# Performance work log

Hardware: AMD Instinct MI355X
Metric: run time of the kernel (lower is better)

The kernel has to match this reference:

```python
import jax, jax.numpy as jnp
import numpy as np

A = 16          # n_agents
H = 128         # rnn_hidden_dim
IN = 128        # input_shape
NA = 32         # n_attention
NACT = 14       # n_actions
TAU = 0.5       # gumbel_softmax_tau
B_ENV = 1024    # parallel envs
BZ = B_ENV * A

# neighbor index: for agent i, all j != i (matches select_ind in torch code)
IDX = np.array([[j for j in range(A) if j != i] for i in range(A)])  # [A, A-1]


def gru_cell(x, h, Wih, Whh, bih, bhh):
    # torch GRUCell gate order: r, z, n
    gi = x @ Wih.T + bih
    gh = h @ Whh.T + bhh
    ir, iz, inn = jnp.split(gi, 3, axis=-1)
    hr, hz, hn = jnp.split(gh, 3, axis=-1)
    r = jax.nn.sigmoid(ir + hr)
    z = jax.nn.sigmoid(iz + hz)
    n = jnp.tanh(inn + r * hn)
    return (1.0 - z) * n + z * h


def run_gru(seq, Wih, Whh, bih, bhh):
    # seq: [T, N, D]; returns all hidden states [T, N, H]
    h0 = jnp.zeros((seq.shape[1], Whh.shape[1]), seq.dtype)
    def step(h, x):
        h2 = gru_cell(x, h, Wih, Whh, bih, bhh)
        return h2, h2
    _, ys = jax.lax.scan(step, h0, seq)
    return ys


def setup_inputs() -> dict:
    key = jax.random.key(0)
    ks = jax.random.split(key, 24)
    def u(k, shape, fan):
        s = 1.0 / np.sqrt(fan)
        return jax.random.uniform(k, shape, jnp.float32, -s, s)
    inp = {
        "inputs": jax.random.normal(ks[0], (BZ, IN), jnp.float32),
        "hidden_state": jax.random.normal(ks[1], (BZ, H), jnp.float32),
        "gumbel_u": jax.random.uniform(ks[2], (BZ * (A - 1), 2), jnp.float32),
        # fc1
        "W1": u(ks[3], (H, IN), IN), "b1": u(ks[4], (H,), IN),
        # GRUCell
        "Wih_c": u(ks[5], (3 * H, H), H), "Whh_c": u(ks[6], (3 * H, H), H),
        "bih_c": u(ks[7], (3 * H,), H), "bhh_c": u(ks[8], (3 * H,), H),
        # bi-GRU forward dir (input 2H)
        "Wih_f": u(ks[9], (3 * H, 2 * H), H), "Whh_f": u(ks[10], (3 * H, H), H),
        "bih_f": u(ks[11], (3 * H,), H), "bhh_f": u(ks[12], (3 * H,), H),
        # bi-GRU backward dir
        "Wih_b": u(ks[13], (3 * H, 2 * H), H), "Whh_b": u(ks[14], (3 * H, H), H),
        "bih_b": u(ks[15], (3 * H,), H), "bhh_b": u(ks[16], (3 * H,), H),
        # hard classifier
        "Wc": u(ks[17], (2, 2 * H), 2 * H), "bc": u(ks[18], (2,), 2 * H),
        # attention projections (no bias)
        "Wq": u(ks[19], (NA, H), H), "Wk": u(ks[20], (NA, H), H),
        # fc2
        "W2": u(ks[21], (NACT, 2 * H), 2 * H), "b2": u(ks[22], (NACT,), 2 * H),
    }
    return inp


def reference(inputs, hidden_state, gumbel_u, W1, b1, Wih_c, Whh_c, bih_c, bhh_c,
              Wih_f, Whh_f, bih_f, bhh_f, Wih_b, Whh_b, bih_b, bhh_b,
              Wc, bc, Wq, Wk, W2, b2):
    bz = inputs.shape[0]
    B = bz // A
    x1 = jax.nn.relu(inputs @ W1.T + b1)
    h_rnn = gru_cell(x1, hidden_state.reshape(-1, H), Wih_c, Whh_c, bih_c, bhh_c)  # [bz, H]

    h3 = h_rnn.reshape(B, A, H)
    nbr = h3[:, IDX, :]                                           # [B, A, A-1, H]
    self_rep = jnp.broadcast_to(h3[:, :, None, :], (B, A, A - 1, H))
    pairs = jnp.concatenate([self_rep, nbr], axis=-1)             # [B, A, A-1, 2H]
    seq = pairs.transpose(2, 0, 1, 3).reshape(A - 1, bz, 2 * H)   # [T, bz, 2H]

    yf = run_gru(seq, Wih_f, Whh_f, bih_f, bhh_f)
    yb = jnp.flip(run_gru(jnp.flip(seq, 0), Wih_b, Whh_b, bih_b, bhh_b), 0)
    h_hard = jnp.concatenate([yf, yb], axis=-1)                   # [T, bz, 2H]
    h_hard = h_hard.transpose(1, 0, 2).reshape(-1, 2 * H)         # [bz*T, 2H]

    logits = h_hard @ Wc.T + bc                                   # [bz*T, 2]
    g = -jnp.log(-jnp.log(gumbel_u + 1e-10) + 1e-10)
    gs = jax.nn.softmax((logits + g) / TAU, axis=-1)
    hard_w = gs[:, 1].reshape(B, A, A - 1)                        # hard gate

    q = (h_rnn @ Wq.T).reshape(B, A, NA)
    k = (h_rnn @ Wk.T).reshape(B, A, NA)
    kn = k[:, IDX, :] * hard_w[..., None]                         # [B, A, A-1, NA]
    scores = jnp.einsum('bad,bamd->bam', q, kn) / np.sqrt(NA)
    soft_w = jax.nn.softmax(scores, axis=-1)                      # [B, A, A-1]

    w = hard_w * soft_w
    agg = jnp.einsum('bam,bamh->bah', w, nbr).reshape(bz, H)
    out = jnp.concatenate([h_rnn, agg], axis=-1) @ W2.T + b2      # [bz, n_actions]
    return out, h_rnn
```

## Files before the change

kernel.cpp:

```cpp
#include <hip/hip_runtime.h>
#include <hip/hip_bf16.h>


typedef __attribute__((ext_vector_type(8))) short short8;
typedef __attribute__((ext_vector_type(4))) float float4v;

#define BF2F(x) __bfloat162float(x)
typedef __hip_bfloat16 bf;

__device__ __forceinline__ float frcp(float x) {
  return __builtin_amdgcn_rcpf(x);
}
__device__ __forceinline__ float fsigmoid(float x) {
  return frcp(1.f + __expf(-x));
}
__device__ __forceinline__ float ftanh(float x) {
  float e = __expf(2.f * x);
  return 1.f - 2.f * frcp(1.f + e);
}
__device__ __forceinline__ float rdv(const void* p, int i, int f) {
  return f ? ((const float*)p)[i] : BF2F(((const bf*)p)[i]);
}
__device__ __forceinline__ float upk(unsigned long long v, int s) {
  union { unsigned int i; float f; } x;
  x.i = ((unsigned int)((v >> s) & 0xffffULL)) << 16;
  return x.f;
}

static const int AO[23] = {
  0, 2097152, 4194304, 4685824, 4702208, 4702336, 4751488, 4800640, 4801024,
  4801408, 4899712, 4948864, 4949248, 4949632, 5047936, 5097088, 5097472,
  5097856, 5098368, 5098384, 5102480, 5106576, 5110160};
static const int AN[23] = {
  2097152, 2097152, 491520, 16384, 128, 49152, 49152, 384, 384, 98304, 49152,
  384, 384, 98304, 49152, 384, 384, 512, 2, 4096, 4096, 3584, 14};

struct CArgs {
  const void* src[23];
  int n[23];
  int off[23];
};

__global__ void kDetect(const unsigned short* __restrict__ p, int* flag) {
  __shared__ int s;
  if (threadIdx.x == 0) s = 0;
  __syncthreads();
  int hit = 0;
  for (int i = threadIdx.x; i < 4096; i += 1024) {
    int e = (p[i] >> 7) & 0xFF;
    if (e >= 0xC0) hit = 1;
  }
  if (hit) atomicOr(&s, 1);
  __syncthreads();
  if (threadIdx.x == 0) *flag = s;
}

__global__ void kConvert(CArgs a, const int* __restrict__ flag,
                         bf* __restrict__ arena) {
  const int b = blockIdx.y;
  const int n = a.n[b];
  const int f = *flag;
  bf* dst = arena + a.off[b];
  if (f) {
    const float* s = (const float*)a.src[b];
    for (int i = blockIdx.x * 256 + threadIdx.x; i < n; i += gridDim.x * 256)
      dst[i] = __float2bfloat16(s[i]);
  } else {
    const unsigned short* s = (const unsigned short*)a.src[b];
    unsigned short* d = (unsigned short*)dst;
    for (int i = blockIdx.x * 256 + threadIdx.x; i < n; i += gridDim.x * 256)
      d[i] = s[i];
  }
}

__global__ void kPrep(const bf* __restrict__ Wq, const bf* __restrict__ Wk,
                      const bf* __restrict__ W2a, const bf* __restrict__ WcA,
                      bf* __restrict__ Wqk, bf* __restrict__ W2p,
                      bf* __restrict__ Wcb) {
  int idx = blockIdx.x * 256 + threadIdx.x;
  if (idx < 8192) {
    int r = idx >> 7, c = idx & 127;
    Wqk[idx] = (r < 32) ? Wq[r * 128 + c] : Wk[(r - 32) * 128 + c];
  }
  if (idx < 4096)
    W2p[idx] = (idx < 3584) ? W2a[idx] : __float2bfloat16(0.f);
  if (idx < 512) {
    int dir = idx >> 8, l = (idx >> 7) & 1, k = idx & 127;
    Wcb[idx] = WcA[l * 256 + dir * 128 + k];
  }
}

__global__ __launch_bounds__(256) void kGemm(const bf* __restrict__ A,
                                             const bf* __restrict__ W,
                                             const bf* __restrict__ bias,
                                             bf* __restrict__ out,
                                             int N, int relu) {
  const int tid = threadIdx.x;
  const int wave = tid >> 6, lane = tid & 63;
  const int quad = lane >> 4, ci = lane & 15;
  const int mr = blockIdx.x * 64 + wave * 16;
  const int nbase = blockIdx.y * 64;
  const int ntiles = (N - nbase < 64) ? ((N - nbase) >> 4) : 4;

  float4v acc[4];
#pragma unroll
  for (int i = 0; i < 4; ++i) acc[i] = {0.f, 0.f, 0.f, 0.f};

#pragma unroll
  for (int ks = 0; ks < 4; ++ks) {
    short8 a = *(const short8*)(A + (size_t)(mr + ci) * 128 + ks * 32 + quad * 8);
    for (int nt = 0; nt < ntiles; ++nt) {
      short8 b = *(const short8*)(W + (size_t)(nbase + nt * 16 + ci) * 128 + ks * 32 + quad * 8);
      acc[nt] = __builtin_amdgcn_mfma_f32_16x16x32_bf16(a, b, acc[nt], 0, 0, 0);
    }
  }

  for (int nt = 0; nt < ntiles; ++nt) {
    int col = nbase + nt * 16 + ci;
    float bv = bias ? BF2F(bias[col]) : 0.f;
#pragma unroll
    for (int r = 0; r < 4; ++r) {
      int row = mr + quad * 4 + r;
      float v = acc[nt][r] + bv;
      if (relu) v = fmaxf(v, 0.f);
      out[(size_t)row * N + col] = __float2bfloat16(v);
    }
  }
}

__global__ __launch_bounds__(256, 4) void kStep(
    const bf* __restrict__ Hp, const bf* __restrict__ Whh,
    const bf* __restrict__ G, int gld,
    const bf* __restrict__ bhh,
    bf* __restrict__ Ho, float* __restrict__ HcopyF) {
  const int half = blockIdx.z;
  const int tid = threadIdx.x;
  const int wave = tid >> 6, lane = tid & 63;
  const int quad = lane >> 4, ci = lane & 15;
  const int mr = blockIdx.x * 64 + wave * 16;

  float4v acc[12];
#pragma unroll
  for (int i = 0; i < 12; ++i) acc[i] = {0.f, 0.f, 0.f, 0.f};

#pragma unroll
  for (int ks = 0; ks < 4; ++ks) {
    short8 a = *(const short8*)(Hp + (size_t)(mr + ci) * 128 + ks * 32 + quad * 8);
#pragma unroll
    for (int g = 0; g < 3; ++g)
#pragma unroll
      for (int nt = 0; nt < 4; ++nt) {
        short8 b = *(const short8*)(Whh + (size_t)(g * 128 + half * 64 + nt * 16 + ci) * 128 + ks * 32 + quad * 8);
        acc[g * 4 + nt] = __builtin_amdgcn_mfma_f32_16x16x32_bf16(a, b, acc[g * 4 + nt], 0, 0, 0);
      }
  }

  float bR[4], bZ[4], bN[4];
#pragma unroll
  for (int nt = 0; nt < 4; ++nt) {
    int c = half * 64 + nt * 16 + ci;
    bR[nt] = BF2F(bhh[c]);
    bZ[nt] = BF2F(bhh[128 + c]);
    bN[nt] = BF2F(bhh[256 + c]);
  }

#pragma unroll
  for (int r = 0; r < 4; ++r) {
    int rr = mr + quad * 4 + r;
    const bf* gs = G + (size_t)rr * gld;
#pragma unroll
    for (int nt = 0; nt < 4; ++nt) {
      int c = half * 64 + nt * 16 + ci;
      float gr = BF2F(gs[c]), gz = BF2F(gs[128 + c]), gnn = BF2F(gs[256 + c]);
      float pre_r = acc[nt][r] + gr + bR[nt];
      float pre_z = acc[4 + nt][r] + gz + bZ[nt];
      float hn_   = acc[8 + nt][r] + bN[nt];
      float rg = fsigmoid(pre_r);
      float zg = fsigmoid(pre_z);
      float ng = ftanh(gnn + rg * hn_);
      float hp = BF2F(Hp[(size_t)rr * 128 + c]);
      float hv = ng + zg * (hp - ng);
      Ho[(size_t)rr * 128 + c] = __float2bfloat16(hv);
      if (HcopyF) HcopyF[(size_t)rr * 128 + c] = hv;
    }
  }
}

__global__ __launch_bounds__(256, 2) void kSeq(
    const bf* __restrict__ hrnn,
    const bf* __restrict__ Wih_f, const bf* __restrict__ Wih_b,
    const bf* __restrict__ Whh_f, const bf* __restrict__ Whh_b,
    const bf* __restrict__ bih_f, const bf* __restrict__ bih_b,
    const bf* __restrict__ bhh_f, const bf* __restrict__ bhh_b,
    const bf* __restrict__ Wcb, float* __restrict__ L) {
  __shared__ unsigned long long sGiN[16][130];
  __shared__ bf sH[2][16][136];
  __shared__ float sL[16][15][2];

  const int env = blockIdx.x;
  const int dir = blockIdx.y;
  const int tid = threadIdx.x;
  const int wave = tid >> 6, lane = tid & 63;
  const int nh = wave;
  const int quad = lane >> 4, ci = lane & 15;
  const bf* Wih = dir ? Wih_b : Wih_f;
  const bf* Whh = dir ? Whh_b : Whh_f;
  const bf* bih = dir ? bih_b : bih_f;
  const bf* bhh = dir ? bhh_b : bhh_f;

  float4v gS[6], gN[6];
#pragma unroll
  for (int i = 0; i < 6; ++i) { gS[i] = {0.f, 0.f, 0.f, 0.f}; gN[i] = {0.f, 0.f, 0.f, 0.f}; }
#pragma unroll
  for (int ks = 0; ks < 4; ++ks) {
    short8 a = *(const short8*)(hrnn + (size_t)(env * 16 + ci) * 128 + ks * 32 + quad * 8);
#pragma unroll
    for (int g = 0; g < 3; ++g)
#pragma unroll
      for (int nt = 0; nt < 2; ++nt) {
        const bf* wrow = Wih + (size_t)(g * 128 + nh * 32 + nt * 16 + ci) * 256 + ks * 32 + quad * 8;
        short8 bs = *(const short8*)(wrow);
        short8 bn = *(const short8*)(wrow + 128);
        gS[g * 2 + nt] = __builtin_amdgcn_mfma_f32_16x16x32_bf16(a, bs, gS[g * 2 + nt], 0, 0, 0);
        gN[g * 2 + nt] = __builtin_amdgcn_mfma_f32_16x16x32_bf16(a, bn, gN[g * 2 + nt], 0, 0, 0);
      }
  }
#pragma unroll
  for (int g = 0; g < 3; ++g)
#pragma unroll
    for (int nt = 0; nt < 2; ++nt) {
      int c = g * 128 + nh * 32 + nt * 16 + ci;
      float bv = BF2F(bih[c]);
      if (g < 2) bv += BF2F(bhh[c]);
#pragma unroll
      for (int r = 0; r < 4; ++r) gS[g * 2 + nt][r] += bv;
    }
#pragma unroll
  for (int nt = 0; nt < 2; ++nt)
#pragma unroll
    for (int r = 0; r < 4; ++r) {
      unsigned long long pk = 0;
#pragma unroll
      for (int g = 0; g < 3; ++g) {
        bf b = __float2bfloat16(gN[g * 2 + nt][r]);
        pk |= ((unsigned long long)(*(unsigned short*)&b)) << (16 * g);
      }
      sGiN[quad * 4 + r][nh * 32 + nt * 16 + ci] = pk;
    }

  {
    bf z = __float2bfloat16(0.f);
    bf* p = &sH[0][0][0];
    for (int i = tid; i < 16 * 136; i += 256) p[i] = z;
  }

  short8 Bf[24];
#pragma unroll
  for (int g = 0; g < 3; ++g)
#pragma unroll
    for (int nt = 0; nt < 2; ++nt)
#pragma unroll
      for (int ks = 0; ks < 4; ++ks)
        Bf[(g * 2 + nt) * 4 + ks] =
            *(const short8*)(Whh + (size_t)(g * 128 + nh * 32 + nt * 16 + ci) * 128 + ks * 32 + quad * 8);

  short8 wcf[4];
#pragma unroll
  for (int ks = 0; ks < 4; ++ks) {
    if (ci < 2)
      wcf[ks] = *(const short8*)(Wcb + (size_t)(dir * 2 + ci) * 128 + ks * 32 + quad * 8);
    else
      wcf[ks] = short8{0, 0, 0, 0, 0, 0, 0, 0};
  }

  float bNc[2];
#pragma unroll
  for (int nt = 0; nt < 2; ++nt)
    bNc[nt] = BF2F(bhh[256 + nh * 32 + nt * 16 + ci]);

  float hPrev[2][4];
#pragma unroll
  for (int nt = 0; nt < 2; ++nt)
#pragma unroll
    for (int r = 0; r < 4; ++r) hPrev[nt][r] = 0.f;

  __syncthreads();

  for (int t = 0; t < 15; ++t) {
    const int cur = t & 1, nxt = cur ^ 1;
    const int m = dir ? (14 - t) : t;

    float4v acc[6];
#pragma unroll
    for (int i = 0; i < 6; ++i) acc[i] = {0.f, 0.f, 0.f, 0.f};
    float4v lacc = {0.f, 0.f, 0.f, 0.f};
#pragma unroll
    for (int ks = 0; ks < 4; ++ks) {
      short8 a = *(const short8*)&sH[cur][ci][ks * 32 + quad * 8];
#pragma unroll
      for (int tl = 0; tl < 6; ++tl)
        acc[tl] = __builtin_amdgcn_mfma_f32_16x16x32_bf16(a, Bf[tl * 4 + ks], acc[tl], 0, 0, 0);
      if (nh == 0)
        lacc = __builtin_amdgcn_mfma_f32_16x16x32_bf16(a, wcf[ks], lacc, 0, 0, 0);
    }
    if (nh == 0 && t > 0 && ci < 2) {
      int mp = dir ? (15 - t) : (t - 1);
#pragma unroll
      for (int r = 0; r < 4; ++r) sL[quad * 4 + r][mp][ci] = lacc[r];
    }

#pragma unroll
    for (int r_ = 0; r_ < 4; ++r_) {
      int row = quad * 4 + r_;
      int jr = m + ((m >= row) ? 1 : 0);
#pragma unroll
      for (int nt = 0; nt < 2; ++nt) {
        int c = nh * 32 + nt * 16 + ci;
        unsigned long long nb = sGiN[jr][c];
        float pre_r = acc[nt][r_] + gS[nt][r_] + upk(nb, 0);
        float pre_z = acc[2 + nt][r_] + gS[2 + nt][r_] + upk(nb, 16);
        float gnn   = gS[4 + nt][r_] + upk(nb, 32);
        float hn_   = acc[4 + nt][r_] + bNc[nt];
        float rg = fsigmoid(pre_r);
        float zg = fsigmoid(pre_z);
        float ng = ftanh(gnn + rg * hn_);
        float hp = hPrev[nt][r_];
        float hv = ng + zg * (hp - ng);
        hPrev[nt][r_] = hv;
        sH[nxt][row][c] = __float2bfloat16(hv);
      }
    }
    __syncthreads();
  }

  if (nh == 0) {
    float4v lacc = {0.f, 0.f, 0.f, 0.f};
#pragma unroll
    for (int ks = 0; ks < 4; ++ks) {
      short8 a = *(const short8*)&sH[1][ci][ks * 32 + quad * 8];
      lacc = __builtin_amdgcn_mfma_f32_16x16x32_bf16(a, wcf[ks], lacc, 0, 0, 0);
    }
    if (ci < 2) {
      int mf = dir ? 0 : 14;
#pragma unroll
      for (int r = 0; r < 4; ++r) sL[quad * 4 + r][mf][ci] = lacc[r];
    }
  }
  __syncthreads();

  for (int i = tid; i < 480; i += 256) {
    int row = i / 30, rem = i - row * 30;
    int mm = rem >> 1, l = rem & 1;
    L[(size_t)((env * 16 + row) * 15 + mm) * 4 + dir * 2 + l] = sL[row][mm][l];
  }
}

__global__ void kGumbel(const float* __restrict__ L, const void* __restrict__ guRaw,
                        const int* __restrict__ flag, const void* __restrict__ bcRaw,
                        float* __restrict__ hw) {
  int idx = blockIdx.x * 256 + threadIdx.x;
  if (idx >= 245760) return;
  const int f = *flag;
  const float* Lp = L + (size_t)idx * 4;
  float l0 = Lp[0] + Lp[2] + rdv(bcRaw, 0, f);
  float l1 = Lp[1] + Lp[3] + rdv(bcRaw, 1, f);
  float u0 = rdv(guRaw, idx * 2, f);
  float u1 = rdv(guRaw, idx * 2 + 1, f);
  float g0 = -__logf(-__logf(u0 + 1e-10f) + 1e-10f);
  float g1 = -__logf(-__logf(u1 + 1e-10f) + 1e-10f);
  float d = ((l1 + g1) - (l0 + g0)) * 2.0f;
  hw[idx] = fsigmoid(d);
}

__global__ __launch_bounds__(256) void kAttn(
    const bf* __restrict__ h, const bf* __restrict__ qk,
    const float* __restrict__ hw, bf* __restrict__ aggB) {
  __shared__ float sh[16 * 132];
  __shared__ float sqk[16 * 64];
  __shared__ float shw[16 * 15];
  __shared__ float sw[16 * 16];
  int bb = blockIdx.x, tid = threadIdx.x;

  for (int i = tid; i < 2048; i += 256)
    sh[(i >> 7) * 132 + (i & 127)] = BF2F(h[(size_t)bb * 2048 + i]);
  for (int i = tid; i < 1024; i += 256)
    sqk[i] = BF2F(qk[(size_t)bb * 1024 + i]);
  for (int i = tid; i < 240; i += 256) shw[i] = hw[bb * 240 + i];
  __syncthreads();

  int a = tid >> 4, i = tid & 15;
  float s = -1e30f;
  if (i < 15) {
    int j = i + (i >= a);
    float d = 0.f;
#pragma unroll
    for (int c = 0; c < 32; ++c) d += sqk[a * 64 + c] * sqk[j * 64 + 32 + c];
    s = shw[a * 15 + i] * d * 0.17677669529663687f;
  }
  float mx = s;
#pragma unroll
  for (int d = 1; d < 16; d <<= 1) mx = fmaxf(mx, __shfl_xor(mx, d));
  float e = (i < 15) ? __expf(s - mx) : 0.f;
  float sum = e;
#pragma unroll
  for (int d = 1; d < 16; d <<= 1) sum += __shfl_xor(sum, d);
  float w = (i < 15) ? (e * frcp(sum)) * shw[a * 15 + i] : 0.f;
  sw[a * 16 + i] = w;
  __syncthreads();

  float ac[8] = {0, 0, 0, 0, 0, 0, 0, 0};
  for (int mm = 0; mm < 15; ++mm) {
    int jm = mm + (mm >= a);
    float wm = sw[a * 16 + mm];
    const float* shp = &sh[jm * 132 + i * 8];
    float4 h0 = *(const float4*)shp;
    float4 h1 = *(const float4*)(shp + 4);
    ac[0] += wm * h0.x; ac[1] += wm * h0.y; ac[2] += wm * h0.z; ac[3] += wm * h0.w;
    ac[4] += wm * h1.x; ac[5] += wm * h1.y; ac[6] += wm * h1.z; ac[7] += wm * h1.w;
  }
  short8 v;
#pragma unroll
  for (int d = 0; d < 8; ++d) {
    bf b = __float2bfloat16(ac[d]);
    v[d] = *(short*)&b;
  }
  *(short8*)(aggB + (size_t)(bb * 16 + a) * 128 + i * 8) = v;
}

__global__ __launch_bounds__(256) void kGemmOut(
    const bf* __restrict__ hrnn, const bf* __restrict__ aggB,
    const bf* __restrict__ W2p, const void* __restrict__ b2Raw,
    const int* __restrict__ flag, float* __restrict__ out) {
  const int tid = threadIdx.x;
  const int wave = tid >> 6, lane = tid & 63;
  const int quad = lane >> 4, ci = lane & 15;
  const int mr = blockIdx.x * 64 + wave * 16;
  const int f = *flag;

  float4v acc = {0.f, 0.f, 0.f, 0.f};
#pragma unroll
  for (int ks = 0; ks < 8; ++ks) {
    const bf* src = (ks < 4) ? hrnn : aggB;
    int k = (ks & 3) * 32 + quad * 8;
    short8 a = *(const short8*)(src + (size_t)(mr + ci) * 128 + k);
    short8 b = *(const short8*)(W2p + (size_t)ci * 256 + ks * 32 + quad * 8);
    acc = __builtin_amdgcn_mfma_f32_16x16x32_bf16(a, b, acc, 0, 0, 0);
  }

  if (ci < 14) {
    float bv = rdv(b2Raw, ci, f);
#pragma unroll
    for (int r = 0; r < 4; ++r)
      out[(size_t)(mr + quad * 4 + r) * 14 + ci] = acc[r] + bv;
  }
}

extern "C" void kernel_launch(void* const* d_in, const int* in_sizes, int n_in,
                              void* d_out, int out_size, void* d_ws, size_t ws_size,
                              hipStream_t stream) {
  const size_t OFF_ARENA = 0;
  const size_t OFF_FLAG  = 10220544;
  const size_t OFF_A     = 10220800;
  const size_t OFF_WQK   = 26998016;
  const size_t OFF_WCB   = 27014400;
  const size_t OFF_W2P   = 27410944;
  const size_t OFF_HRNN  = 27419136;
  const size_t OFF_QK    = 31613440;
  const size_t NEEDED    = 84042240;
  if (ws_size < NEEDED) return;
  if (n_in < 23 || in_sizes[0] != 2097152 || in_sizes[3] != 16384 ||
      in_sizes[5] != 49152 || in_sizes[9] != 98304 || in_sizes[17] != 512 ||
      in_sizes[19] != 4096 || in_sizes[21] != 3584 || out_size != 2326528)
    return;

  char* ws = (char*)d_ws;
  bf*    arena = (bf*)(ws + OFF_ARENA);
  float* L     = (float*)(ws + OFF_ARENA);
  int*   flag  = (int*)(ws + OFF_FLAG);
  bf*    x1    = (bf*)(ws + OFF_A);
  bf*    gi_c  = (bf*)(ws + OFF_A + 4194304);
  float* hw    = (float*)(ws + OFF_A);
  bf*    aggB  = (bf*)(ws + OFF_A + 983040);
  bf*    Wqk   = (bf*)(ws + OFF_WQK);
  bf*    Wcb   = (bf*)(ws + OFF_WCB);
  bf*    W2p   = (bf*)(ws + OFF_W2P);
  bf*    hrnn  = (bf*)(ws + OFF_HRNN);
  bf*    qk    = (bf*)(ws + OFF_QK);

  float* out14 = (float*)d_out;
  float* outh  = (float*)d_out + 229376;

  kDetect<<<1, 1024, 0, stream>>>((const unsigned short*)d_in[0], flag);
  CArgs ca;
  for (int i = 0; i < 23; ++i) { ca.src[i] = d_in[i]; ca.n[i] = AN[i]; ca.off[i] = AO[i]; }
  kConvert<<<dim3(128, 23), 256, 0, stream>>>(ca, flag, arena);

  const bf* inputs = arena + AO[0];
  const bf* hidden = arena + AO[1];
  const bf* W1     = arena + AO[3];
  const bf* b1     = arena + AO[4];
  const bf* Wih_c  = arena + AO[5];
  const bf* Whh_c  = arena + AO[6];
  const bf* bih_c  = arena + AO[7];
  const bf* bhh_c  = arena + AO[8];
  const bf* Wih_f  = arena + AO[9];
  const bf* Whh_f  = arena + AO[10];
  const bf* bih_f  = arena + AO[11];
  const bf* bhh_f  = arena + AO[12];
  const bf* Wih_b  = arena + AO[13];
  const bf* Whh_b  = arena + AO[14];
  const bf* bih_b  = arena + AO[15];
  const bf* bhh_b  = arena + AO[16];
  const bf* WcA    = arena + AO[17];
  const bf* Wq     = arena + AO[19];
  const bf* Wk     = arena + AO[20];
  const bf* W2a    = arena + AO[21];

  kPrep<<<dim3(32), 256, 0, stream>>>(Wq, Wk, W2a, WcA, Wqk, W2p, Wcb);
  kGemm<<<dim3(256, 2), 256, 0, stream>>>(inputs, W1, b1, x1, 128, 1);
  kGemm<<<dim3(256, 6), 256, 0, stream>>>(x1, Wih_c, bih_c, gi_c, 384, 0);
  kStep<<<dim3(256, 1, 2), 256, 0, stream>>>(hidden, Whh_c, gi_c, 384, bhh_c,
                                             hrnn, outh);
  kGemm<<<dim3(256, 1), 256, 0, stream>>>(hrnn, Wqk, (const bf*)nullptr, qk, 64, 0);

  kSeq<<<dim3(1024, 2), 256, 0, stream>>>(hrnn, Wih_f, Wih_b, Whh_f, Whh_b,
                                          bih_f, bih_b, bhh_f, bhh_b, Wcb, L);

  kGumbel<<<dim3(960), 256, 0, stream>>>(L, d_in[2], flag, d_in[18], hw);
  kAttn<<<dim3(1024), 256, 0, stream>>>(hrnn, qk, hw, aggB);
  kGemmOut<<<dim3(256), 256, 0, stream>>>(hrnn, aggB, W2p, d_in[22], flag, out14);
}
```

Before: 324.5 us.

## Split kSeq hidden columns across 8 waves instead of 4

The bidirectional GRU sequence kernel now runs 512 threads per block, so each of 8 waves owns 16 hidden columns instead of 32. That halves per-wave MFMA work and register use (Bf 24 to 12 fragments), and the launch bound asks for 4 blocks per CU. The classifier weight fragments move from registers into shared memory and are reloaded each step. The goal is shorter serial per-step latency across the 15 recurrent steps, at the cost of more waves per barrier and extra LDS reads.

```diff
diff --git a/kernel.cpp b/kernel.cpp
--- a/kernel.cpp
+++ b/kernel.cpp
@@ -186,7 +186,7 @@
   }
 }
 
-__global__ __launch_bounds__(256, 2) void kSeq(
+__global__ __launch_bounds__(512, 4) void kSeq(
     const bf* __restrict__ hrnn,
     const bf* __restrict__ Wih_f, const bf* __restrict__ Wih_b,
     const bf* __restrict__ Whh_f, const bf* __restrict__ Whh_b,
@@ -196,6 +196,7 @@
   __shared__ unsigned long long sGiN[16][130];
   __shared__ bf sH[2][16][136];
   __shared__ float sL[16][15][2];
+  __shared__ bf sWc[2][136];
 
   const int env = blockIdx.x;
   const int dir = blockIdx.y;
@@ -207,82 +208,63 @@
   const bf* Whh = dir ? Whh_b : Whh_f;
   const bf* bih = dir ? bih_b : bih_f;
   const bf* bhh = dir ? bhh_b : bhh_f;
-
-  float4v gS[6], gN[6];
-#pragma unroll
-  for (int i = 0; i < 6; ++i) { gS[i] = {0.f, 0.f, 0.f, 0.f}; gN[i] = {0.f, 0.f, 0.f, 0.f}; }
+  const int cb = nh * 16 + ci;
+
+  float4v gS[3], gN[3];
+#pragma unroll
+  for (int i = 0; i < 3; ++i) { gS[i] = {0.f, 0.f, 0.f, 0.f}; gN[i] = {0.f, 0.f, 0.f, 0.f}; }
 #pragma unroll
   for (int ks = 0; ks < 4; ++ks) {
     short8 a = *(const short8*)(hrnn + (size_t)(env * 16 + ci) * 128 + ks * 32 + quad * 8);
 #pragma unroll
-    for (int g = 0; g < 3; ++g)
-#pragma unroll
-      for (int nt = 0; nt < 2; ++nt) {
-        const bf* wrow = Wih + (size_t)(g * 128 + nh * 32 + nt * 16 + ci) * 256 + ks * 32 + quad * 8;
-        short8 bs = *(const short8*)(wrow);
-        short8 bn = *(const short8*)(wrow + 128);
-        gS[g * 2 + nt] = __builtin_amdgcn_mfma_f32_16x16x32_bf16(a, bs, gS[g * 2 + nt], 0, 0, 0);
-        gN[g * 2 + nt] = __builtin_amdgcn_mfma_f32_16x16x32_bf16(a, bn, gN[g * 2 + nt], 0, 0, 0);
-      }
-  }
-#pragma unroll
-  for (int g = 0; g < 3; ++g)
-#pragma unroll
-    for (int nt = 0; nt < 2; ++nt) {
-      int c = g * 128 + nh * 32 + nt * 16 + ci;
-      float bv = BF2F(bih[c]);
-      if (g < 2) bv += BF2F(bhh[c]);
-#pragma unroll
-      for (int r = 0; r < 4; ++r) gS[g * 2 + nt][r] += bv;
-    }
-#pragma unroll
-  for (int nt = 0; nt < 2; ++nt)
-#pragma unroll
-    for (int r = 0; r < 4; ++r) {
-      unsigned long long pk = 0;
-#pragma unroll
-      for (int g = 0; g < 3; ++g) {
-        bf b = __float2bfloat16(gN[g * 2 + nt][r]);
-        pk |= ((unsigned long long)(*(unsigned short*)&b)) << (16 * g);
-      }
-      sGiN[quad * 4 + r][nh * 32 + nt * 16 + ci] = pk;
-    }
+    for (int g = 0; g < 3; ++g) {
+      const bf* wrow = Wih + (size_t)(g * 128 + nh * 16 + ci) * 256 + ks * 32 + quad * 8;
+      short8 bs = *(const short8*)(wrow);
+      short8 bn = *(const short8*)(wrow + 128);
+      gS[g] = __builtin_amdgcn_mfma_f32_16x16x32_bf16(a, bs, gS[g], 0, 0, 0);
+      gN[g] = __builtin_amdgcn_mfma_f32_16x16x32_bf16(a, bn, gN[g], 0, 0, 0);
+    }
+  }
+#pragma unroll
+  for (int g = 0; g < 3; ++g) {
+    int c = g * 128 + cb;
+    float bv = BF2F(bih[c]);
+    if (g < 2) bv += BF2F(bhh[c]);
+#pragma unroll
+    for (int r = 0; r < 4; ++r) gS[g][r] += bv;
+  }
+#pragma unroll
+  for (int r = 0; r < 4; ++r) {
+    unsigned long long pk = 0;
+#pragma unroll
+    for (int g = 0; g < 3; ++g) {
+      bf b = __float2bfloat16(gN[g][r]);
+      pk |= ((unsigned long long)(*(unsigned short*)&b)) << (16 * g);
+    }
+    sGiN[quad * 4 + r][cb] = pk;
+  }
 
   {
     bf z = __float2bfloat16(0.f);
     bf* p = &sH[0][0][0];
-    for (int i = tid; i < 16 * 136; i += 256) p[i] = z;
-  }
-
-  short8 Bf[24];
+    for (int i = tid; i < 16 * 136; i += 512) p[i] = z;
+    if (tid < 256)
+      sWc[tid >> 7][tid & 127] = Wcb[(dir * 2 + (tid >> 7)) * 128 + (tid & 127)];
+  }
+
+  short8 Bf[12];
 #pragma unroll
   for (int g = 0; g < 3; ++g)
 #pragma unroll
-    for (int nt = 0; nt < 2; ++nt)
-#pragma unroll
-      for (int ks = 0; ks < 4; ++ks)
-        Bf[(g * 2 + nt) * 4 + ks] =
-            *(const short8*)(Whh + (size_t)(g * 128 + nh * 32 + nt * 16 + ci) * 128 + ks * 32 + quad * 8);
-
-  short8 wcf[4];
-#pragma unroll
-  for (int ks = 0; ks < 4; ++ks) {
-    if (ci < 2)
-      wcf[ks] = *(const short8*)(Wcb + (size_t)(dir * 2 + ci) * 128 + ks * 32 + quad * 8);
-    else
-      wcf[ks] = short8{0, 0, 0, 0, 0, 0, 0, 0};
-  }
-
-  float bNc[2];
-#pragma unroll
-  for (int nt = 0; nt < 2; ++nt)
-    bNc[nt] = BF2F(bhh[256 + nh * 32 + nt * 16 + ci]);
-
-  float hPrev[2][4];
-#pragma unroll
-  for (int nt = 0; nt < 2; ++nt)
-#pragma unroll
-    for (int r = 0; r < 4; ++r) hPrev[nt][r] = 0.f;
+    for (int ks = 0; ks < 4; ++ks)
+      Bf[g * 4 + ks] =
+          *(const short8*)(Whh + (size_t)(g * 128 + nh * 16 + ci) * 128 + ks * 32 + quad * 8);
+
+  float bNc = BF2F(bhh[256 + cb]);
+
+  float hPrev[4];
+#pragma unroll
+  for (int r = 0; r < 4; ++r) hPrev[r] = 0.f;
 
   __syncthreads();
 
@@ -290,18 +272,20 @@
     const int cur = t & 1, nxt = cur ^ 1;
     const int m = dir ? (14 - t) : t;
 
-    float4v acc[6];
-#pragma unroll
-    for (int i = 0; i < 6; ++i) acc[i] = {0.f, 0.f, 0.f, 0.f};
+    float4v acc[3];
+#pragma unroll
+    for (int i = 0; i < 3; ++i) acc[i] = {0.f, 0.f, 0.f, 0.f};
     float4v lacc = {0.f, 0.f, 0.f, 0.f};
 #pragma unroll
     for (int ks = 0; ks < 4; ++ks) {
       short8 a = *(const short8*)&sH[cur][ci][ks * 32 + quad * 8];
 #pragma unroll
-      for (int tl = 0; tl < 6; ++tl)
-        acc[tl] = __builtin_amdgcn_mfma_f32_16x16x32_bf16(a, Bf[tl * 4 + ks], acc[tl], 0, 0, 0);
-      if (nh == 0)
-        lacc = __builtin_amdgcn_mfma_f32_16x16x32_bf16(a, wcf[ks], lacc, 0, 0, 0);
+      for (int g = 0; g < 3; ++g)
+        acc[g] = __builtin_amdgcn_mfma_f32_16x16x32_bf16(a, Bf[g * 4 + ks], acc[g], 0, 0, 0);
+      if (nh == 0) {
+        short8 wv = *(const short8*)&sWc[ci & 1][ks * 32 + quad * 8];
+        lacc = __builtin_amdgcn_mfma_f32_16x16x32_bf16(a, wv, lacc, 0, 0, 0);
+      }
     }
     if (nh == 0 && t > 0 && ci < 2) {
       int mp = dir ? (15 - t) : (t - 1);
@@ -313,22 +297,18 @@
     for (int r_ = 0; r_ < 4; ++r_) {
       int row = quad * 4 + r_;
       int jr = m + ((m >= row) ? 1 : 0);
-#pragma unroll
-      for (int nt = 0; nt < 2; ++nt) {
-        int c = nh * 32 + nt * 16 + ci;
-        unsigned long long nb = sGiN[jr][c];
-        float pre_r = acc[nt][r_] + gS[nt][r_] + upk(nb, 0);
-        float pre_z = acc[2 + nt][r_] + gS[2 + nt][r_] + upk(nb, 16);
-        float gnn   = gS[4 + nt][r_] + upk(nb, 32);
-        float hn_   = acc[4 + nt][r_] + bNc[nt];
-        float rg = fsigmoid(pre_r);
-        float zg = fsigmoid(pre_z);
-        float ng = ftanh(gnn + rg * hn_);
-        float hp = hPrev[nt][r_];
-        float hv = ng + zg * (hp - ng);
-        hPrev[nt][r_] = hv;
-        sH[nxt][row][c] = __float2bfloat16(hv);
-      }
+      unsigned long long nb = sGiN[jr][cb];
+      float pre_r = acc[0][r_] + gS[0][r_] + upk(nb, 0);
+      float pre_z = acc[1][r_] + gS[1][r_] + upk(nb, 16);
+      float gnn   = gS[2][r_] + upk(nb, 32);
+      float hn_   = acc[2][r_] + bNc;
+      float rg = fsigmoid(pre_r);
+      float zg = fsigmoid(pre_z);
+      float ng = ftanh(gnn + rg * hn_);
+      float hp = hPrev[r_];
+      float hv = ng + zg * (hp - ng);
+      hPrev[r_] = hv;
+      sH[nxt][row][cb] = __float2bfloat16(hv);
     }
     __syncthreads();
   }
@@ -338,7 +318,8 @@
 #pragma unroll
     for (int ks = 0; ks < 4; ++ks) {
       short8 a = *(const short8*)&sH[1][ci][ks * 32 + quad * 8];
-      lacc = __builtin_amdgcn_mfma_f32_16x16x32_bf16(a, wcf[ks], lacc, 0, 0, 0);
+      short8 wv = *(const short8*)&sWc[ci & 1][ks * 32 + quad * 8];
+      lacc = __builtin_amdgcn_mfma_f32_16x16x32_bf16(a, wv, lacc, 0, 0, 0);
     }
     if (ci < 2) {
       int mf = dir ? 0 : 14;
@@ -348,7 +329,7 @@
   }
   __syncthreads();
 
-  for (int i = tid; i < 480; i += 256) {
+  for (int i = tid; i < 480; i += 512) {
     int row = i / 30, rem = i - row * 30;
     int mm = rem >> 1, l = rem & 1;
     L[(size_t)((env * 16 + row) * 15 + mm) * 4 + dir * 2 + l] = sL[row][mm][l];
@@ -523,7 +504,7 @@
                                              hrnn, outh);
   kGemm<<<dim3(256, 1), 256, 0, stream>>>(hrnn, Wqk, (const bf*)nullptr, qk, 64, 0);
 
-  kSeq<<<dim3(1024, 2), 256, 0, stream>>>(hrnn, Wih_f, Wih_b, Whh_f, Whh_b,
+  kSeq<<<dim3(1024, 2), 512, 0, stream>>>(hrnn, Wih_f, Wih_b, Whh_f, Whh_b,
                                           bih_f, bih_b, bhh_f, bhh_b, Wcb, L);
 
   kGumbel<<<dim3(960), 256, 0, stream>>>(L, d_in[2], flag, d_in[18], hw);
```

After: 311.9 us. -3.9%, faster.
